# Performance work log

Measured on AMD Instinct MI355X. Metric: run time of the kernel, lower is better.

Reference implementation:

```python
import jax, jax.numpy as jnp
import numpy as np

TAIL_BOUND = 20.0  # B
NUM_BINS = 16      # K
G, I = 8, 64       # n_gaussians, n_inputs
BATCH = 16384


def _rqs_forward(x, W, H, D, B):
    """Monotonic rational-quadratic spline (Durkan et al.), forward direction.
    x: [Bt,G,I]; W,H: [G,I,K] logits; D: [G,I,K-1] raw derivatives.
    Matches torch module: widths/heights = 2*B*softmax(logits), derivs = softplus,
    boundary derivatives fixed to 1, identity outside [-B, B].
    """
    dt = x.dtype
    widths = 2.0 * B * jax.nn.softmax(W, axis=-1)          # [G,I,K], sums to 2B
    heights = 2.0 * B * jax.nn.softmax(H, axis=-1)
    g, i, K = widths.shape
    one = jnp.ones((g, i, 1), dt)
    derivs = jnp.concatenate([one, jax.nn.softplus(D), one], axis=-1)  # [G,I,K+1]
    negB = jnp.full((g, i, 1), -B, dt)
    cumw = jnp.concatenate([negB, -B + jnp.cumsum(widths, -1)], -1)    # [G,I,K+1] knot x
    cumh = jnp.concatenate([negB, -B + jnp.cumsum(heights, -1)], -1)   # [G,I,K+1] knot y
    delta = heights / widths                                            # bin slopes

    inside = (x >= -B) & (x <= B)
    xc = jnp.clip(x, -B, B)
    # bin search: index of bin containing xc (broadcast compare vs. K+1 knots)
    idx = jnp.clip(jnp.sum((xc[..., None] >= cumw[None]).astype(jnp.int32), axis=-1) - 1, 0, K - 1)  # [Bt,G,I]

    gi = jnp.arange(g)[:, None]
    ii = jnp.arange(i)[None, :]

    def gather(p, j):  # p: [G,I,*], j: [Bt,G,I] -> [Bt,G,I]
        return p[gi, ii, j]

    in_cw, in_w = gather(cumw, idx), gather(widths, idx)
    in_ch, in_h = gather(cumh, idx), gather(heights, idx)
    in_delta = gather(delta, idx)
    d0, d1 = gather(derivs, idx), gather(derivs, idx + 1)

    theta = (xc - in_cw) / in_w
    tt = theta * (1.0 - theta)
    denom = in_delta + (d0 + d1 - 2.0 * in_delta) * tt
    numer = in_h * (in_delta * theta * theta + d0 * tt)
    z_in = in_ch + numer / denom
    dnum = in_delta * in_delta * (d1 * theta * theta + 2.0 * in_delta * tt + d0 * (1.0 - theta) ** 2)
    ld_in = jnp.log(dnum) - 2.0 * jnp.log(denom)

    z = jnp.where(inside, z_in, x)
    ld = jnp.where(inside, ld_in, jnp.zeros((), dt))
    return z, ld


def setup_inputs() -> dict:
    key = jax.random.key(0)
    kx, kw, kh, kd = jax.random.split(key, 4)
    # scale x so points spread across many bins; a few land outside the tail bound
    x = jax.random.normal(kx, (BATCH, G, I), dtype=jnp.float32) * 12.0
    W = jax.random.normal(kw, (G, I, NUM_BINS), dtype=jnp.float32)
    H = jax.random.normal(kh, (G, I, NUM_BINS), dtype=jnp.float32)
    D = jax.random.normal(kd, (G, I, NUM_BINS - 1), dtype=jnp.float32)
    return {"x": x, "W": W, "H": H, "D": D}


def reference(x, W, H, D):
    return _rqs_forward(x, W, H, D, TAIL_BOUND)
```

## Files before the change

### kernel.cpp

```cpp
#include <hip/hip_runtime.h>
#include <math.h>

#define TAIL_B 20.0f
#define GI 512
#define BATCH 16384
#define NELEM (BATCH * GI)
#define ROWS_PB 64

typedef float vf4 __attribute__((ext_vector_type(4)));

#define G_KNT 0
#define G_CW  960
#define G_CH  2048
#define G_DK  3136
#define GSTRIDE 4224
#define LDSF 3264

__global__ __launch_bounds__(256) void rqs_precompute(
    const float* __restrict__ W, const float* __restrict__ H,
    const float* __restrict__ D, float* __restrict__ ws)
{
    int gi = blockIdx.x * 256 + threadIdx.x;
    if (gi >= GI) return;
    int g = gi >> 6, il = gi & 63;
    float* bg = ws + g * GSTRIDE;

    const float* Wg = W + gi * 16;
    const float* Hg = H + gi * 16;
    const float* Dg = D + gi * 15;

    float mw = Wg[0], mh = Hg[0];
#pragma unroll
    for (int k = 1; k < 16; ++k) { mw = fmaxf(mw, Wg[k]); mh = fmaxf(mh, Hg[k]); }
    float sumw = 0.0f, sumh = 0.0f;
#pragma unroll
    for (int k = 0; k < 16; ++k) { sumw += expf(Wg[k] - mw); sumh += expf(Hg[k] - mh); }
    float scw = (2.0f * TAIL_B) / sumw;
    float sch = (2.0f * TAIL_B) / sumh;

    bg[G_CW + il * 17] = -TAIL_B;
    bg[G_CH + il * 17] = -TAIL_B;
    bg[G_DK + il * 17] = 1.0f;

    float cw = -TAIL_B, ch = -TAIL_B;
#pragma unroll
    for (int k = 0; k < 16; ++k) {
        float wk = expf(Wg[k] - mw) * scw;
        float hk = expf(Hg[k] - mh) * sch;
        cw += wk; ch += hk;
        float dnext = 1.0f;
        if (k < 15) {
            float v = Dg[k];
            dnext = fmaxf(v, 0.0f) + log1pf(expf(-fabsf(v)));
        }
        bg[G_CW + il * 17 + k + 1] = cw;
        bg[G_CH + il * 17 + k + 1] = ch;
        bg[G_DK + il * 17 + k + 1] = dnext;
        if (k < 15) bg[G_KNT + k * 64 + il] = cw;
    }
}

__global__ __launch_bounds__(256, 8) void rqs_main(
    const float* __restrict__ x, const float* __restrict__ ws,
    float* __restrict__ out)
{
    __shared__ float s[LDSF];

    int g     = blockIdx.x & 7;
    int chunk = blockIdx.x >> 3;
    int lane  = threadIdx.x & 63;
    int wsub  = threadIdx.x >> 6;

    const float* bg = ws + g * GSTRIDE;

    int colbase = g * 64 + lane;
    int rowbase = chunk * ROWS_PB + wsub;

    float xb[16];
#pragma unroll
    for (int i = 0; i < 16; ++i)
        xb[i] = x[(rowbase + i * 4) * 512 + colbase];

    {
        const vf4* src = reinterpret_cast<const vf4*>(bg + G_CW);
        vf4*       dst = reinterpret_cast<vf4*>(s);
#pragma unroll
        for (int i = 0; i < 4; ++i) {
            int t = threadIdx.x + 256 * i;
            if (t < LDSF / 4) dst[t] = src[t];
        }
    }

    float kr[15];
#pragma unroll
    for (int t = 0; t < 15; ++t) kr[t] = bg[G_KNT + t * 64 + lane];

    __syncthreads();

    const float* sCW = s;
    const float* sCH = s + 1088;
    const float* sDK = s + 2176;

#pragma unroll
    for (int i = 0; i < 16; ++i) {
        float xx = xb[i];
        bool  inside = (xx >= -TAIL_B) && (xx <= TAIL_B);
        float xc = fminf(fmaxf(xx, -TAIL_B), TAIL_B);

        int idx = 0;
#pragma unroll
        for (int t = 0; t < 15; ++t) idx += (xc >= kr[t]) ? 1 : 0;

        int p = lane * 17 + idx;
        float k0  = sCW[p], k1  = sCW[p + 1];
        float ch0 = sCH[p], ch1 = sCH[p + 1];
        float d0  = sDK[p], d1  = sDK[p + 1];

        float invw  = __builtin_amdgcn_rcpf(k1 - k0);
        float hh    = ch1 - ch0;
        float de    = hh * invw;
        float theta = (xc - k0) * invw;
        float omt   = 1.0f - theta;
        float tt    = theta * omt;
        float denom = de + (d0 + d1 - 2.0f * de) * tt;
        float rden  = __builtin_amdgcn_rcpf(denom);
        float numer = hh * (de * theta * theta + d0 * tt);
        float zin   = ch0 + numer * rden;
        float dnum  = de * de * (d1 * theta * theta + 2.0f * de * tt + d0 * omt * omt);
        float ldin  = 0.6931471805599453f * __log2f(dnum * rden * rden);

        float z  = inside ? zin : xx;
        float ld = inside ? ldin : 0.0f;

        int addr = (rowbase + i * 4) * 512 + colbase;
        __builtin_nontemporal_store(z,  out + addr);
        __builtin_nontemporal_store(ld, out + NELEM + addr);
    }
}

extern "C" void kernel_launch(void* const* d_in, const int* in_sizes, int n_in,
                              void* d_out, int out_size, void* d_ws, size_t ws_size,
                              hipStream_t stream)
{
    const float* x = (const float*)d_in[0];
    const float* W = (const float*)d_in[1];
    const float* H = (const float*)d_in[2];
    const float* D = (const float*)d_in[3];
    float* out = (float*)d_out;
    float* ws  = (float*)d_ws;

    rqs_precompute<<<GI / 256, 256, 0, stream>>>(W, H, D, ws);

    int nblocks = 8 * (BATCH / ROWS_PB);
    rqs_main<<<nblocks, 256, 0, stream>>>(x, ws, out);
}
```

Measured before the change: 31.93 us.

## Fuse spline parameter precompute into main kernel, computing per-block in LDS

```diff
diff --git a/kernel.cpp b/kernel.cpp
--- a/kernel.cpp
+++ b/kernel.cpp
@@ -9,69 +9,20 @@
 
 typedef float vf4 __attribute__((ext_vector_type(4)));
 
-#define G_KNT 0
-#define G_CW  960
-#define G_CH  2048
-#define G_DK  3136
-#define GSTRIDE 4224
 #define LDSF 3264
 
-__global__ __launch_bounds__(256) void rqs_precompute(
-    const float* __restrict__ W, const float* __restrict__ H,
-    const float* __restrict__ D, float* __restrict__ ws)
-{
-    int gi = blockIdx.x * 256 + threadIdx.x;
-    if (gi >= GI) return;
-    int g = gi >> 6, il = gi & 63;
-    float* bg = ws + g * GSTRIDE;
-
-    const float* Wg = W + gi * 16;
-    const float* Hg = H + gi * 16;
-    const float* Dg = D + gi * 15;
-
-    float mw = Wg[0], mh = Hg[0];
-#pragma unroll
-    for (int k = 1; k < 16; ++k) { mw = fmaxf(mw, Wg[k]); mh = fmaxf(mh, Hg[k]); }
-    float sumw = 0.0f, sumh = 0.0f;
-#pragma unroll
-    for (int k = 0; k < 16; ++k) { sumw += expf(Wg[k] - mw); sumh += expf(Hg[k] - mh); }
-    float scw = (2.0f * TAIL_B) / sumw;
-    float sch = (2.0f * TAIL_B) / sumh;
-
-    bg[G_CW + il * 17] = -TAIL_B;
-    bg[G_CH + il * 17] = -TAIL_B;
-    bg[G_DK + il * 17] = 1.0f;
-
-    float cw = -TAIL_B, ch = -TAIL_B;
-#pragma unroll
-    for (int k = 0; k < 16; ++k) {
-        float wk = expf(Wg[k] - mw) * scw;
-        float hk = expf(Hg[k] - mh) * sch;
-        cw += wk; ch += hk;
-        float dnext = 1.0f;
-        if (k < 15) {
-            float v = Dg[k];
-            dnext = fmaxf(v, 0.0f) + log1pf(expf(-fabsf(v)));
-        }
-        bg[G_CW + il * 17 + k + 1] = cw;
-        bg[G_CH + il * 17 + k + 1] = ch;
-        bg[G_DK + il * 17 + k + 1] = dnext;
-        if (k < 15) bg[G_KNT + k * 64 + il] = cw;
-    }
-}
-
-__global__ __launch_bounds__(256, 8) void rqs_main(
-    const float* __restrict__ x, const float* __restrict__ ws,
+__global__ __launch_bounds__(256, 8) void rqs_fused(
+    const float* __restrict__ x, const float* __restrict__ W,
+    const float* __restrict__ H, const float* __restrict__ D,
     float* __restrict__ out)
 {
     __shared__ float s[LDSF];
 
+    int tid   = threadIdx.x;
     int g     = blockIdx.x & 7;
     int chunk = blockIdx.x >> 3;
-    int lane  = threadIdx.x & 63;
-    int wsub  = threadIdx.x >> 6;
-
-    const float* bg = ws + g * GSTRIDE;
+    int lane  = tid & 63;
+    int wsub  = tid >> 6;
 
     int colbase = g * 64 + lane;
     int rowbase = chunk * ROWS_PB + wsub;
@@ -82,20 +33,70 @@
         xb[i] = x[(rowbase + i * 4) * 512 + colbase];
 
     {
-        const vf4* src = reinterpret_cast<const vf4*>(bg + G_CW);
-        vf4*       dst = reinterpret_cast<vf4*>(s);
+        int col = tid >> 2;
+        int kp  = tid & 3;
+        int gi  = g * 64 + col;
+        int qb  = lane & ~3;
+
+        vf4 wv = *reinterpret_cast<const vf4*>(W + gi * 16 + kp * 4);
+        vf4 hv = *reinterpret_cast<const vf4*>(H + gi * 16 + kp * 4);
+
+        float mw = fmaxf(fmaxf(wv.x, wv.y), fmaxf(wv.z, wv.w));
+        float mh = fmaxf(fmaxf(hv.x, hv.y), fmaxf(hv.z, hv.w));
+        mw = fmaxf(mw, __shfl_xor(mw, 1)); mw = fmaxf(mw, __shfl_xor(mw, 2));
+        mh = fmaxf(mh, __shfl_xor(mh, 1)); mh = fmaxf(mh, __shfl_xor(mh, 2));
+
+        float w0 = expf(wv.x - mw), w1 = expf(wv.y - mw),
+              w2 = expf(wv.z - mw), w3 = expf(wv.w - mw);
+        float h0 = expf(hv.x - mh), h1 = expf(hv.y - mh),
+              h2 = expf(hv.z - mh), h3 = expf(hv.w - mh);
+        float Tw = w0 + w1 + w2 + w3;
+        float Th = h0 + h1 + h2 + h3;
+
+        float tw0 = __shfl(Tw, qb), tw1 = __shfl(Tw, qb + 1),
+              tw2 = __shfl(Tw, qb + 2), tw3 = __shfl(Tw, qb + 3);
+        float th0 = __shfl(Th, qb), th1 = __shfl(Th, qb + 1),
+              th2 = __shfl(Th, qb + 2), th3 = __shfl(Th, qb + 3);
+        float scw = (2.0f * TAIL_B) / (tw0 + tw1 + tw2 + tw3);
+        float sch = (2.0f * TAIL_B) / (th0 + th1 + th2 + th3);
+        float offw = (kp > 0 ? tw0 : 0.f) + (kp > 1 ? tw1 : 0.f) + (kp > 2 ? tw2 : 0.f);
+        float offh = (kp > 0 ? th0 : 0.f) + (kp > 1 ? th1 : 0.f) + (kp > 2 ? th2 : 0.f);
+
+        float cwb = -TAIL_B + offw * scw;
+        float chb = -TAIL_B + offh * sch;
+
+        float* sc = s + col * 17;
+        sc[4 * kp + 1]        = cwb + w0 * scw;
+        sc[4 * kp + 2]        = cwb + (w0 + w1) * scw;
+        sc[4 * kp + 3]        = cwb + (w0 + w1 + w2) * scw;
+        sc[4 * kp + 4]        = cwb + (w0 + w1 + w2 + w3) * scw;
+        sc[1088 + 4 * kp + 1] = chb + h0 * sch;
+        sc[1088 + 4 * kp + 2] = chb + (h0 + h1) * sch;
+        sc[1088 + 4 * kp + 3] = chb + (h0 + h1 + h2) * sch;
+        sc[1088 + 4 * kp + 4] = chb + (h0 + h1 + h2 + h3) * sch;
+
+        const float* Dg = D + gi * 15;
 #pragma unroll
-        for (int i = 0; i < 4; ++i) {
-            int t = threadIdx.x + 256 * i;
-            if (t < LDSF / 4) dst[t] = src[t];
+        for (int j = 0; j < 4; ++j) {
+            int t = 4 * kp + 1 + j;
+            float dv = 1.0f;
+            if (t < 16) {
+                float v = Dg[t - 1];
+                dv = fmaxf(v, 0.0f) + log1pf(expf(-fabsf(v)));
+            }
+            sc[2176 + t] = dv;
+        }
+        if (kp == 0) {
+            sc[0]    = -TAIL_B;
+            sc[1088] = -TAIL_B;
+            sc[2176] = 1.0f;
         }
     }
+    __syncthreads();
 
     float kr[15];
 #pragma unroll
-    for (int t = 0; t < 15; ++t) kr[t] = bg[G_KNT + t * 64 + lane];
-
-    __syncthreads();
+    for (int t = 0; t < 15; ++t) kr[t] = s[lane * 17 + 1 + t];
 
     const float* sCW = s;
     const float* sCH = s + 1088;
@@ -147,10 +148,7 @@
     const float* H = (const float*)d_in[2];
     const float* D = (const float*)d_in[3];
     float* out = (float*)d_out;
-    float* ws  = (float*)d_ws;
-
-    rqs_precompute<<<GI / 256, 256, 0, stream>>>(W, H, D, ws);
 
     int nblocks = 8 * (BATCH / ROWS_PB);
-    rqs_main<<<nblocks, 256, 0, stream>>>(x, ws, out);
+    rqs_fused<<<nblocks, 256, 0, stream>>>(x, W, H, D, out);
 }
```

Result: faster. 30.99 us (-2.9%).
